# Performance work log

Hardware: AMD Instinct MI355X
Metric: run time of the kernel (lower is better)

The kernel has to match this reference:

```python
import jax, jax.numpy as jnp
import numpy as np

N = 100_000      # nodes
E = 1_600_000    # graph edges
M = 10_000       # hyperedges
I = 800_000      # hypergraph incidences
F_IN = 128
HID = 128


def _lin(key, fan_in, fan_out):
    return (jax.random.normal(key, (fan_in, fan_out), jnp.float32) / np.sqrt(fan_in)).astype(jnp.float32)


def setup_inputs() -> dict:
    key = jax.random.key(0)
    ks = jax.random.split(key, 14)
    x = jax.random.normal(ks[0], (N, F_IN), jnp.float32)
    edge_index = jax.random.randint(ks[1], (2, E), 0, N, dtype=jnp.int32)
    edge_weights = jax.random.uniform(ks[2], (E,), jnp.float32)
    node_idx = jax.random.randint(ks[3], (I,), 0, N, dtype=jnp.int32)
    he_idx = jax.random.randint(ks[4], (I,), 0, M, dtype=jnp.int32)
    hyperedge_index = jnp.stack([node_idx, he_idx])
    hyperedge_distances = jax.random.uniform(ks[5], (M,), jnp.float32)
    return {
        "x": x,
        "edge_index": edge_index,
        "edge_weights": edge_weights,
        "hyperedge_index": hyperedge_index,
        "hyperedge_distances": hyperedge_distances,
        "W_g1": _lin(ks[6], F_IN, HID), "b_g1": jnp.zeros((HID,), jnp.float32),
        "W_g2": _lin(ks[7], HID, HID), "b_g2": jnp.zeros((HID,), jnp.float32),
        "W_h1": _lin(ks[8], F_IN, HID), "b_h1": jnp.zeros((HID,), jnp.float32),
        "W_h2": _lin(ks[9], HID, HID), "b_h2": jnp.zeros((HID,), jnp.float32),
        "W_fc": _lin(ks[10], 2 * HID, HID), "b_fc": jnp.zeros((HID,), jnp.float32),
        "W_out": _lin(ks[11], HID, 2), "b_out": jnp.zeros((2,), jnp.float32),
    }


def _gcn(h_in, W, b, row, col, ew):
    # PyG GCNConv: lin -> sym-normalized scatter-add (self-loops included in row/col/ew) -> +bias
    h = h_in @ W
    deg = jax.ops.segment_sum(ew, col, num_segments=N)
    dis = jnp.where(deg > 0, jax.lax.rsqrt(deg), 0.0)
    norm = dis[row] * ew * dis[col]
    out = jax.ops.segment_sum(norm[:, None] * h[row], col, num_segments=N)
    return out + b


def _hyper(h_in, W, b, node_idx, he_idx):
    # PyG HypergraphConv (use_attention=False, hyperedge_weight=1):
    # out = D^{-1} H B^{-1} H^T (X W) + b
    h = h_in @ W
    D = jax.ops.segment_sum(jnp.ones((node_idx.shape[0],), h.dtype), node_idx, num_segments=N)
    Dinv = jnp.where(D > 0, 1.0 / D, 0.0)
    Bc = jax.ops.segment_sum(jnp.ones((he_idx.shape[0],), h.dtype), he_idx, num_segments=M)
    Binv = jnp.where(Bc > 0, 1.0 / Bc, 0.0)
    edge_feat = Binv[:, None] * jax.ops.segment_sum(h[node_idx], he_idx, num_segments=M)
    out = Dinv[:, None] * jax.ops.segment_sum(edge_feat[he_idx], node_idx, num_segments=N)
    return out + b


def reference(x, edge_index, edge_weights, hyperedge_index, hyperedge_distances,
              W_g1, b_g1, W_g2, b_g2, W_h1, b_h1, W_h2, b_h2,
              W_fc, b_fc, W_out, b_out):
    # add self-loops (GCNConv default add_self_loops=True, fill=1)
    loops = jnp.arange(N, dtype=edge_index.dtype)
    row = jnp.concatenate([edge_index[0], loops])
    col = jnp.concatenate([edge_index[1], loops])
    ew = jnp.concatenate([edge_weights, jnp.ones((N,), edge_weights.dtype)])

    # GCN branch (dropout = identity in eval)
    x1 = jax.nn.relu(_gcn(x, W_g1, b_g1, row, col, ew))
    x1 = jax.nn.relu(_gcn(x1, W_g2, b_g2, row, col, ew))

    # vectorized form of the per-incidence python loop:
    # node_hyperedge_weights[v] = sum over incidences (v, e) of hyperedge_distances[e]
    node_idx, he_idx = hyperedge_index[0], hyperedge_index[1]
    nhw = jax.ops.segment_sum(hyperedge_distances[he_idx], node_idx, num_segments=N)
    x2 = x * nhw[:, None]

    x2 = jax.nn.relu(_hyper(x2, W_h1, b_h1, node_idx, he_idx))
    x2 = jax.nn.relu(_hyper(x2, W_h2, b_h2, node_idx, he_idx))

    h = jnp.concatenate([x1, x2], axis=1)
    h = jax.nn.relu(h @ W_fc + b_fc)
    return h @ W_out + b_out
```

## Files before the change

kernel.cpp:

```cpp
#include <hip/hip_runtime.h>
#include <hip/hip_fp16.h>


#define THREADS 256
#define CAP_E  64
#define CAP_IN 40
#define CAP_IH 144

#define BC_E 4608
#define BC_I 2432
#define BC_H 3072

#define P1_ITEMS 16
#define P1_BLOCK 4096

#define SMEM_MM 50176

typedef _Float16 half8 __attribute__((ext_vector_type(8)));
typedef float floatx4 __attribute__((ext_vector_type(4)));

#define FIX_SCALE 16777216.0f

template <int MODE>
__device__ __forceinline__ void phase1_core(
    int blk, const int* __restrict__ keys, const int* __restrict__ vals,
    const float* __restrict__ wts,
    unsigned long long* __restrict__ buf64, unsigned int* __restrict__ buf32,
    int* __restrict__ bincnt, int nitems, int nbins, int bincap,
    unsigned int* hist, unsigned int* off, unsigned int* gb, unsigned int* wsum,
    unsigned long long* reord, unsigned short* rbin) {
  const int tid = threadIdx.x;
  const int base = blk * P1_BLOCK;
  for (int i = tid; i < 512; i += 256) hist[i] = 0;
  __syncthreads();
  unsigned long long pl[P1_ITEMS];
  int bn[P1_ITEMS], lr[P1_ITEMS];
#pragma unroll
  for (int j = 0; j < P1_ITEMS; ++j) {
    int idx = base + j * 256 + tid;
    bn[j] = -1;
    if (idx < nitems) {
      int k = keys[idx], v = vals[idx];
      if (MODE == 0) {
        bn[j] = k >> 8;
        pl[j] = ((unsigned long long)__float_as_uint(wts[idx]) << 32) |
                ((unsigned long long)((unsigned int)v << 8)) |
                (unsigned long long)(k & 255);
      } else if (MODE == 1) {
        bn[j] = k >> 8;
        pl[j] = (unsigned long long)(((unsigned int)v << 8) | (unsigned int)(k & 255));
      } else {
        bn[j] = k >> 5;
        pl[j] = (unsigned long long)(((unsigned int)v << 5) | (unsigned int)(k & 31));
      }
      lr[j] = (int)atomicAdd(&hist[bn[j]], 1u);
    }
  }
  __syncthreads();
  unsigned int v0 = hist[2 * tid], v1 = hist[2 * tid + 1];
  unsigned int tsum = v0 + v1;
  unsigned int incl = tsum;
  for (int o = 1; o < 64; o <<= 1) {
    unsigned int t = __shfl_up(incl, o, 64);
    if ((tid & 63) >= o) incl += t;
  }
  if ((tid & 63) == 63) wsum[tid >> 6] = incl;
  __syncthreads();
  unsigned int woff = 0;
  for (int w = 0; w < (tid >> 6); ++w) woff += wsum[w];
  unsigned int texcl = incl - tsum + woff;
  off[2 * tid] = texcl;
  off[2 * tid + 1] = texcl + v0;
  if (2 * tid < nbins && v0) gb[2 * tid] = (unsigned int)atomicAdd(&bincnt[2 * tid], (int)v0);
  if (2 * tid + 1 < nbins && v1) gb[2 * tid + 1] = (unsigned int)atomicAdd(&bincnt[2 * tid + 1], (int)v1);
  __syncthreads();
#pragma unroll
  for (int j = 0; j < P1_ITEMS; ++j) {
    if (bn[j] >= 0) {
      unsigned int pos = off[bn[j]] + (unsigned int)lr[j];
      reord[pos] = pl[j];
      rbin[pos] = (unsigned short)bn[j];
    }
  }
  __syncthreads();
  int total = nitems - base;
  if (total > P1_BLOCK) total = P1_BLOCK;
#pragma unroll
  for (int j = 0; j < P1_ITEMS; ++j) {
    int p = j * 256 + tid;
    if (p < total) {
      int b = rbin[p];
      unsigned int idx = gb[b] + (unsigned int)p - off[b];
      if (idx < (unsigned int)bincap) {
        if (MODE == 0) buf64[(size_t)b * bincap + idx] = reord[p];
        else buf32[(size_t)b * bincap + idx] = (unsigned int)reord[p];
      }
    }
  }
}

__global__ __launch_bounds__(256) void bin_phase1_all(
    const int* __restrict__ col, const int* __restrict__ row, const float* __restrict__ ew,
    const int* __restrict__ vidx, const int* __restrict__ heidx,
    unsigned long long* __restrict__ buf_e, unsigned int* __restrict__ buf_in,
    unsigned int* __restrict__ buf_ih,
    int* __restrict__ bincnt_e, int* __restrict__ bincnt_in, int* __restrict__ bincnt_ih,
    int E, int I, int GB_E, int GB_I, int NB_E, int NB_I, int NB_H) {
  __shared__ unsigned int hist[512];
  __shared__ unsigned int off[512];
  __shared__ unsigned int gb[512];
  __shared__ unsigned int wsum[4];
  __shared__ unsigned long long reord[P1_BLOCK];
  __shared__ unsigned short rbin[P1_BLOCK];
  int b = blockIdx.x;
  if (b < GB_E)
    phase1_core<0>(b, col, row, ew, buf_e, nullptr, bincnt_e, E, NB_E, BC_E,
                   hist, off, gb, wsum, reord, rbin);
  else if (b < GB_E + GB_I)
    phase1_core<1>(b - GB_E, vidx, heidx, nullptr, nullptr, buf_in, bincnt_in, I, NB_I, BC_I,
                   hist, off, gb, wsum, reord, rbin);
  else
    phase1_core<2>(b - GB_E - GB_I, heidx, vidx, nullptr, nullptr, buf_ih, bincnt_ih, I, NB_H, BC_H,
                   hist, off, gb, wsum, reord, rbin);
}

__global__ __launch_bounds__(256) void bin_phase2_all(
    const unsigned long long* __restrict__ buf_e, const unsigned int* __restrict__ buf_in,
    const unsigned int* __restrict__ buf_ih,
    const int* __restrict__ bincnt_e, const int* __restrict__ bincnt_in,
    const int* __restrict__ bincnt_ih, const float* __restrict__ hd,
    int2* __restrict__ epairs, int* __restrict__ he_by_node, int* __restrict__ v_by_he,
    int* __restrict__ ecnt, float* __restrict__ dis,
    int* __restrict__ ncnt, float* __restrict__ nhwf, float* __restrict__ Dinv,
    int* __restrict__ hecnt, float* __restrict__ Binv,
    int N, int M, int NB_E, int NB_I) {
  __shared__ unsigned int cnt[256];
  __shared__ unsigned int aux[256];
  const int tid = threadIdx.x;
  int b = blockIdx.x;
  if (b < NB_E) {
    cnt[tid] = 0; aux[tid] = 0;
    __syncthreads();
    int tot = bincnt_e[b]; if (tot > BC_E) tot = BC_E;
    const unsigned long long* seg = buf_e + (size_t)b * BC_E;
    for (int i = tid; i < tot; i += 256) {
      unsigned long long pl = seg[i];
      int c_lo = (int)(pl & 255u);
      int r = (int)((pl >> 8) & 0xFFFFFFu);
      float w = __uint_as_float((unsigned int)(pl >> 32));
      unsigned int s = atomicAdd(&cnt[c_lo], 1u);
      atomicAdd(&aux[c_lo], (unsigned int)(w * FIX_SCALE + 0.5f));
      if (s < CAP_E)
        epairs[((size_t)b * 256 + c_lo) * CAP_E + s] = make_int2(r, __float_as_int(w));
    }
    __syncthreads();
    int v = b * 256 + tid;
    if (v < N) {
      unsigned int c = cnt[tid];
      ecnt[v] = (c < CAP_E) ? (int)c : CAP_E;
      dis[v] = rsqrtf(1.0f + (float)aux[tid] * (1.0f / FIX_SCALE));
    }
  } else if (b < NB_E + NB_I) {
    b -= NB_E;
    cnt[tid] = 0; aux[tid] = 0;
    __syncthreads();
    int tot = bincnt_in[b]; if (tot > BC_I) tot = BC_I;
    const unsigned int* seg = buf_in + (size_t)b * BC_I;
    for (int i = tid; i < tot; i += 256) {
      unsigned int pl = seg[i];
      int v_lo = (int)(pl & 255u);
      int e = (int)(pl >> 8);
      unsigned int s = atomicAdd(&cnt[v_lo], 1u);
      atomicAdd(&aux[v_lo], (unsigned int)(hd[e] * FIX_SCALE + 0.5f));
      if (s < CAP_IN) he_by_node[((size_t)b * 256 + v_lo) * CAP_IN + s] = e;
    }
    __syncthreads();
    int v = b * 256 + tid;
    if (v < N) {
      unsigned int c = cnt[tid];
      ncnt[v] = (c < CAP_IN) ? (int)c : CAP_IN;
      nhwf[v] = (float)aux[tid] * (1.0f / FIX_SCALE);
      Dinv[v] = (c > 0) ? 1.0f / (float)c : 0.0f;
    }
  } else {
    b -= NB_E + NB_I;
    if (tid < 32) cnt[tid] = 0;
    __syncthreads();
    int tot = bincnt_ih[b]; if (tot > BC_H) tot = BC_H;
    const unsigned int* seg = buf_ih + (size_t)b * BC_H;
    for (int i = tid; i < tot; i += 256) {
      unsigned int pl = seg[i];
      int e_lo = (int)(pl & 31u);
      int v = (int)(pl >> 5);
      unsigned int s = atomicAdd(&cnt[e_lo], 1u);
      if (s < CAP_IH) v_by_he[((size_t)b * 32 + e_lo) * CAP_IH + s] = v;
    }
    __syncthreads();
    if (tid < 32) {
      int e = b * 32 + tid;
      if (e < M) {
        unsigned int c = cnt[tid];
        hecnt[e] = (c < CAP_IH) ? (int)c : CAP_IH;
        Binv[e] = (c > 0) ? 1.0f / (float)c : 0.0f;
      }
    }
  }
}

__global__ void prep_k(const float* __restrict__ Wg1, const float* __restrict__ Wg2,
                       const float* __restrict__ Wh1, const float* __restrict__ Wh2,
                       const float* __restrict__ Wfc,
                       _Float16* __restrict__ Wtg1, _Float16* __restrict__ Wtg2,
                       _Float16* __restrict__ Wth1, _Float16* __restrict__ Wth2,
                       _Float16* __restrict__ Wtfc, int* __restrict__ bincnt, int nbins) {
  if (blockIdx.x == gridDim.x - 1) {
    for (int i = threadIdx.x; i < nbins; i += 256) bincnt[i] = 0;
    return;
  }
  int idx = blockIdx.x * THREADS + threadIdx.x;
  if (idx < 65536) {
    int s = idx >> 14, local = idx & 16383;
    const float* W = (s == 0) ? Wg1 : (s == 1) ? Wg2 : (s == 2) ? Wh1 : Wh2;
    _Float16* Wt = (s == 0) ? Wtg1 : (s == 1) ? Wtg2 : (s == 2) ? Wth1 : Wth2;
    int n = local >> 7, kk = local & 127;
    int k = kk ^ ((n & 7) << 3);
    Wt[local] = (_Float16)W[k * 128 + n];
  } else if (idx < 98304) {
    int local = idx - 65536;
    int n = local >> 8, kk = local & 255;
    int k = kk ^ ((n & 7) << 3);
    Wtfc[local] = (_Float16)Wfc[k * 128 + n];
  }
}

__device__ __forceinline__ void mm_core(
    int blk, const _Float16* __restrict__ A, const _Float16* __restrict__ Wt,
    const float* __restrict__ scale, _Float16* __restrict__ Cout, int nrows,
    unsigned char* smem) {
  _Float16* WtL = (_Float16*)smem;
  _Float16* ebuf = (_Float16*)(smem + 32768);
  const int tid = threadIdx.x;
  {
    const float4* src = (const float4*)Wt;
    float4* dst = (float4*)WtL;
#pragma unroll
    for (int i = 0; i < 8; ++i) dst[tid + 256 * i] = src[tid + 256 * i];
  }
  __syncthreads();
  const int w = tid >> 6, l = tid & 63;
  const int m = l & 15, quad = l >> 4;
  const int rbase = blk * 256 + w * 64;
  floatx4 acc[4][8];
#pragma unroll
  for (int r = 0; r < 4; ++r)
#pragma unroll
    for (int c = 0; c < 8; ++c)
#pragma unroll
      for (int j = 0; j < 4; ++j) acc[r][c][j] = 0.0f;
#pragma unroll
  for (int s = 0; s < 4; ++s) {
    const int ks = s * 32 + quad * 8;
    half8 a[4];
#pragma unroll
    for (int r = 0; r < 4; ++r) {
      int gr = rbase + r * 16 + m;
      if (gr < nrows) {
        a[r] = *(const half8*)(A + (size_t)gr * 128 + ks);
      } else {
#pragma unroll
        for (int j = 0; j < 8; ++j) a[r][j] = (_Float16)0.0f;
      }
    }
#pragma unroll
    for (int c = 0; c < 8; ++c) {
      int n = c * 16 + m;
      half8 b = *(const half8*)&WtL[n * 128 + (ks ^ ((n & 7) << 3))];
#pragma unroll
      for (int r = 0; r < 4; ++r)
        acc[r][c] = __builtin_amdgcn_mfma_f32_16x16x32_f16(a[r], b, acc[r][c], 0, 0, 0);
    }
  }
  _Float16* eb = ebuf + w * (16 * 136);
#pragma unroll
  for (int r = 0; r < 4; ++r) {
    float dv[4];
#pragma unroll
    for (int j = 0; j < 4; ++j) {
      int grow = rbase + r * 16 + quad * 4 + j;
      dv[j] = (scale && grow < nrows) ? scale[grow] : 1.0f;
    }
#pragma unroll
    for (int c = 0; c < 8; ++c)
#pragma unroll
      for (int j = 0; j < 4; ++j)
        eb[(quad * 4 + j) * 136 + c * 16 + m] = (_Float16)(acc[r][c][j] * dv[j]);
#pragma unroll
    for (int t = 0; t < 4; ++t) {
      int chunk = t * 64 + l;
      int rr = chunk >> 4;
      int off = (chunk & 15) * 8;
      int gr = rbase + r * 16 + rr;
      half8 v = *(const half8*)&eb[rr * 136 + off];
      if (gr < nrows) *(half8*)(Cout + (size_t)gr * 128 + off) = v;
    }
  }
}

__global__ __launch_bounds__(256) void mm_dual(
    const float* __restrict__ X, const _Float16* __restrict__ Wt1,
    const _Float16* __restrict__ Wt2, _Float16* __restrict__ C1,
    _Float16* __restrict__ C2, int nrows) {
  __shared__ __align__(16) unsigned char smem[SMEM_MM];
  _Float16* WtL = (_Float16*)smem;
  _Float16* ebuf = (_Float16*)(smem + 32768);
  const int tid = threadIdx.x;
  const int w = tid >> 6, l = tid & 63;
  const int m = l & 15, quad = l >> 4;
  const int rbase = blockIdx.x * 256 + w * 64;
  half8 a[4][4];
#pragma unroll
  for (int r = 0; r < 4; ++r) {
    int gr = rbase + r * 16 + m;
#pragma unroll
    for (int s = 0; s < 4; ++s) {
      int ks = s * 32 + quad * 8;
      if (gr < nrows) {
        float4 f0 = *(const float4*)(X + (size_t)gr * 128 + ks);
        float4 f1 = *(const float4*)(X + (size_t)gr * 128 + ks + 4);
        half8 h;
        h[0] = (_Float16)f0.x; h[1] = (_Float16)f0.y; h[2] = (_Float16)f0.z; h[3] = (_Float16)f0.w;
        h[4] = (_Float16)f1.x; h[5] = (_Float16)f1.y; h[6] = (_Float16)f1.z; h[7] = (_Float16)f1.w;
        a[r][s] = h;
      } else {
#pragma unroll
        for (int j = 0; j < 8; ++j) a[r][s][j] = (_Float16)0.0f;
      }
    }
  }
  _Float16* eb = ebuf + w * (16 * 136);
  for (int pass = 0; pass < 2; ++pass) {
    {
      const float4* src = (const float4*)(pass ? Wt2 : Wt1);
      float4* dst = (float4*)WtL;
#pragma unroll
      for (int i = 0; i < 8; ++i) dst[tid + 256 * i] = src[tid + 256 * i];
    }
    __syncthreads();
    floatx4 acc[4][8];
#pragma unroll
    for (int r = 0; r < 4; ++r)
#pragma unroll
      for (int c = 0; c < 8; ++c)
#pragma unroll
        for (int j = 0; j < 4; ++j) acc[r][c][j] = 0.0f;
#pragma unroll
    for (int s = 0; s < 4; ++s) {
      const int ks = s * 32 + quad * 8;
#pragma unroll
      for (int c = 0; c < 8; ++c) {
        int n = c * 16 + m;
        half8 b = *(const half8*)&WtL[n * 128 + (ks ^ ((n & 7) << 3))];
#pragma unroll
        for (int r = 0; r < 4; ++r)
          acc[r][c] = __builtin_amdgcn_mfma_f32_16x16x32_f16(a[r][s], b, acc[r][c], 0, 0, 0);
      }
    }
    _Float16* Cout = pass ? C2 : C1;
#pragma unroll
    for (int r = 0; r < 4; ++r) {
#pragma unroll
      for (int c = 0; c < 8; ++c)
#pragma unroll
        for (int j = 0; j < 4; ++j)
          eb[(quad * 4 + j) * 136 + c * 16 + m] = (_Float16)acc[r][c][j];
#pragma unroll
      for (int t = 0; t < 4; ++t) {
        int chunk = t * 64 + l;
        int rr = chunk >> 4;
        int off = (chunk & 15) * 8;
        int gr = rbase + r * 16 + rr;
        half8 v = *(const half8*)&eb[rr * 136 + off];
        if (gr < nrows) *(half8*)(Cout + (size_t)gr * 128 + off) = v;
      }
    }
    __syncthreads();
  }
}

__global__ __launch_bounds__(256) void mm_pair(
    const _Float16* __restrict__ A1, const _Float16* __restrict__ Wt1,
    const float* __restrict__ scale1, _Float16* __restrict__ C1,
    const _Float16* __restrict__ A2, const _Float16* __restrict__ Wt2,
    _Float16* __restrict__ C2, int nrows, int GMM) {
  __shared__ __align__(16) unsigned char smem[SMEM_MM];
  int b = blockIdx.x;
  if (b < GMM) mm_core(b, A1, Wt1, scale1, C1, nrows, smem);
  else         mm_core(b - GMM, A2, Wt2, nullptr, C2, nrows, smem);
}

template <int PRESCALED>
__device__ __forceinline__ void gcn_core(
    int blk, const _Float16* __restrict__ h, const int* __restrict__ ecnt,
    const int2* __restrict__ epairs, const float* __restrict__ dis,
    const float* __restrict__ bias, _Float16* __restrict__ out, int N) {
  int g = threadIdx.x >> 4, l = threadIdx.x & 15;
  int c = blk * 16 + g;
  if (c >= N) return;
  const float4* h4 = (const float4*)h;
  float dc = dis[c];
  float4 self = h4[(size_t)c * 16 + l];
  const _Float16* sp = (const _Float16*)&self;
  float acc[8];
#pragma unroll
  for (int j = 0; j < 8; ++j) acc[j] = PRESCALED ? (float)sp[j] : dc * (float)sp[j];
  int cnt = ecnt[c];
  const int2* seg = epairs + (size_t)c * CAP_E;
  int p = 0;
  for (; p + 2 <= cnt; p += 2) {
    int2 pr0 = seg[p];
    int2 pr1 = seg[p + 1];
    float4 hv0 = h4[(size_t)pr0.x * 16 + l];
    float4 hv1 = h4[(size_t)pr1.x * 16 + l];
    float w0 = __int_as_float(pr0.y), w1 = __int_as_float(pr1.y);
    if (!PRESCALED) { w0 *= dis[pr0.x]; w1 *= dis[pr1.x]; }
    const _Float16* hp0 = (const _Float16*)&hv0;
    const _Float16* hp1 = (const _Float16*)&hv1;
#pragma unroll
    for (int j = 0; j < 8; ++j) acc[j] = fmaf(w0, (float)hp0[j], acc[j]);
#pragma unroll
    for (int j = 0; j < 8; ++j) acc[j] = fmaf(w1, (float)hp1[j], acc[j]);
  }
  if (p < cnt) {
    int2 pr = seg[p];
    float wgt = __int_as_float(pr.y);
    if (!PRESCALED) wgt *= dis[pr.x];
    float4 hv = h4[(size_t)pr.x * 16 + l];
    const _Float16* hp = (const _Float16*)&hv;
#pragma unroll
    for (int j = 0; j < 8; ++j) acc[j] = fmaf(wgt, (float)hp[j], acc[j]);
  }
  float4 b0 = ((const float4*)bias)[2 * l];
  float4 b1 = ((const float4*)bias)[2 * l + 1];
  float bb[8] = {b0.x, b0.y, b0.z, b0.w, b1.x, b1.y, b1.z, b1.w};
  half8 ov;
#pragma unroll
  for (int j = 0; j < 8; ++j) ov[j] = (_Float16)fmaxf(fmaf(acc[j], dc, bb[j]), 0.f);
  *(half8*)(out + (size_t)c * 128 + l * 8) = ov;
}

template <int SCALED>
__device__ __forceinline__ void hyperef_core(
    int blk, const _Float16* __restrict__ h, const int* __restrict__ hecnt,
    const int* __restrict__ v_by_he, const float* __restrict__ Binv,
    const float* __restrict__ nhwf, _Float16* __restrict__ ef, int M) {
  int g = threadIdx.x >> 4, l = threadIdx.x & 15;
  int e = blk * 16 + g;
  if (e >= M) return;
  const float4* h4 = (const float4*)h;
  float acc[8];
#pragma unroll
  for (int j = 0; j < 8; ++j) acc[j] = 0.f;
  int cnt = hecnt[e];
  const int* seg = v_by_he + (size_t)e * CAP_IH;
  int p = 0;
  for (; p + 4 <= cnt; p += 4) {
    int v0 = seg[p], v1 = seg[p + 1], v2 = seg[p + 2], v3 = seg[p + 3];
    float4 a0 = h4[(size_t)v0 * 16 + l];
    float4 a1 = h4[(size_t)v1 * 16 + l];
    float4 a2 = h4[(size_t)v2 * 16 + l];
    float4 a3 = h4[(size_t)v3 * 16 + l];
    float s0 = 1.f, s1 = 1.f, s2 = 1.f, s3 = 1.f;
    if (SCALED) { s0 = nhwf[v0]; s1 = nhwf[v1]; s2 = nhwf[v2]; s3 = nhwf[v3]; }
    const _Float16* p0 = (const _Float16*)&a0;
    const _Float16* p1 = (const _Float16*)&a1;
    const _Float16* p2 = (const _Float16*)&a2;
    const _Float16* p3 = (const _Float16*)&a3;
    if (SCALED) {
#pragma unroll
      for (int j = 0; j < 8; ++j)
        acc[j] += s0 * (float)p0[j] + s1 * (float)p1[j] + s2 * (float)p2[j] + s3 * (float)p3[j];
    } else {
#pragma unroll
      for (int j = 0; j < 8; ++j)
        acc[j] += ((float)p0[j] + (float)p1[j]) + ((float)p2[j] + (float)p3[j]);
    }
  }
  for (; p < cnt; ++p) {
    int v = seg[p];
    float4 hv = h4[(size_t)v * 16 + l];
    const _Float16* hp = (const _Float16*)&hv;
    if (SCALED) {
      float s = nhwf[v];
#pragma unroll
      for (int j = 0; j < 8; ++j) acc[j] = fmaf(s, (float)hp[j], acc[j]);
    } else {
#pragma unroll
      for (int j = 0; j < 8; ++j) acc[j] += (float)hp[j];
    }
  }
  float bi = Binv[e];
  half8 ov;
#pragma unroll
  for (int j = 0; j < 8; ++j) ov[j] = (_Float16)(acc[j] * bi);
  *(half8*)(ef + (size_t)e * 128 + l * 8) = ov;
}

__global__ __launch_bounds__(256) void g_he_1(
    const _Float16* __restrict__ Bg, const int* __restrict__ ecnt,
    const int2* __restrict__ epairs, const float* __restrict__ dis,
    const float* __restrict__ bg1, _Float16* __restrict__ Bt1,
    const _Float16* __restrict__ Bh, const int* __restrict__ hecnt,
    const int* __restrict__ v_by_he, const float* __restrict__ Binv,
    const float* __restrict__ nhwf, _Float16* __restrict__ ef,
    int N, int M, int GN16) {
  int b = blockIdx.x;
  if (b < GN16) gcn_core<0>(b, Bg, ecnt, epairs, dis, bg1, Bt1, N);
  else hyperef_core<1>(b - GN16, Bh, hecnt, v_by_he, Binv, nhwf, ef, M);
}

__global__ __launch_bounds__(256) void g_he_2(
    const _Float16* __restrict__ Btmp1, const int* __restrict__ ecnt,
    const int2* __restrict__ epairs, const float* __restrict__ dis,
    const float* __restrict__ bg2, _Float16* __restrict__ Bt1,
    const _Float16* __restrict__ Btmp2, const int* __restrict__ hecnt,
    const int* __restrict__ v_by_he, const float* __restrict__ Binv,
    _Float16* __restrict__ ef, int N, int M, int GN16) {
  int b = blockIdx.x;
  if (b < GN16) gcn_core<1>(b, Btmp1, ecnt, epairs, dis, bg2, Bt1, N);
  else hyperef_core<0>(b - GN16, Btmp2, hecnt, v_by_he, Binv, nullptr, ef, M);
}

__global__ __launch_bounds__(256) void hyper_out16(
    const _Float16* __restrict__ ef, const int* __restrict__ ncnt,
    const int* __restrict__ he_by_node, const float* __restrict__ Dinv,
    const float* __restrict__ bias, _Float16* __restrict__ out, int N) {
  int g = threadIdx.x >> 4, l = threadIdx.x & 15;
  int v = blockIdx.x * 16 + g;
  if (v >= N) return;
  const float4* ef4 = (const float4*)ef;
  float acc[8];
#pragma unroll
  for (int j = 0; j < 8; ++j) acc[j] = 0.f;
  int cnt = ncnt[v];
  const int* seg = he_by_node + (size_t)v * CAP_IN;
  int p = 0;
  for (; p + 2 <= cnt; p += 2) {
    int e0 = seg[p], e1 = seg[p + 1];
    float4 a0 = ef4[(size_t)e0 * 16 + l];
    float4 a1 = ef4[(size_t)e1 * 16 + l];
    const _Float16* p0 = (const _Float16*)&a0;
    const _Float16* p1 = (const _Float16*)&a1;
#pragma unroll
    for (int j = 0; j < 8; ++j) acc[j] += (float)p0[j] + (float)p1[j];
  }
  if (p < cnt) {
    int e = seg[p];
    float4 hv = ef4[(size_t)e * 16 + l];
    const _Float16* hp = (const _Float16*)&hv;
#pragma unroll
    for (int j = 0; j < 8; ++j) acc[j] += (float)hp[j];
  }
  float di = Dinv[v];
  float4 b0 = ((const float4*)bias)[2 * l];
  float4 b1 = ((const float4*)bias)[2 * l + 1];
  float bb[8] = {b0.x, b0.y, b0.z, b0.w, b1.x, b1.y, b1.z, b1.w};
  half8 ov;
#pragma unroll
  for (int j = 0; j < 8; ++j) ov[j] = (_Float16)fmaxf(fmaf(acc[j], di, bb[j]), 0.f);
  *(half8*)(out + (size_t)v * 128 + l * 8) = ov;
}

__global__ __launch_bounds__(256) void fc_head(
    const _Float16* __restrict__ A1, const _Float16* __restrict__ A2,
    const _Float16* __restrict__ Wt, const float* __restrict__ bfc,
    const float* __restrict__ Wout, const float* __restrict__ bout,
    float* __restrict__ out, int nrows) {
  __shared__ _Float16 WtL[128 * 128];
  __shared__ float WoutL[256];
  const int tid = threadIdx.x;
  WoutL[tid] = Wout[tid];
  const int w = tid >> 6, l = tid & 63;
  const int m = l & 15, quad = l >> 4;
  const int rbase = blockIdx.x * 256 + w * 64;
  floatx4 acc[4][8];
#pragma unroll
  for (int r = 0; r < 4; ++r)
#pragma unroll
    for (int c = 0; c < 8; ++c)
#pragma unroll
      for (int j = 0; j < 4; ++j) acc[r][c][j] = 0.0f;
  for (int half = 0; half < 2; ++half) {
    {
      const float4* src = (const float4*)Wt;
      float4* dst = (float4*)WtL;
#pragma unroll
      for (int i = 0; i < 8; ++i) {
        int idx = tid + 256 * i;
        dst[idx] = src[(idx >> 4) * 32 + half * 16 + (idx & 15)];
      }
    }
    __syncthreads();
    const _Float16* Asrc = half ? A2 : A1;
#pragma unroll
    for (int ss = 0; ss < 4; ++ss) {
      const int kl = ss * 32 + quad * 8;
      half8 a[4];
#pragma unroll
      for (int r = 0; r < 4; ++r) {
        int gr = rbase + r * 16 + m;
        if (gr < nrows) {
          a[r] = *(const half8*)(Asrc + (size_t)gr * 128 + kl);
        } else {
#pragma unroll
          for (int j = 0; j < 8; ++j) a[r][j] = (_Float16)0.0f;
        }
      }
#pragma unroll
      for (int c = 0; c < 8; ++c) {
        int n = c * 16 + m;
        half8 b = *(const half8*)&WtL[n * 128 + (kl ^ ((n & 7) << 3))];
#pragma unroll
        for (int r = 0; r < 4; ++r)
          acc[r][c] = __builtin_amdgcn_mfma_f32_16x16x32_f16(a[r], b, acc[r][c], 0, 0, 0);
      }
    }
    __syncthreads();
  }
  float b0 = bout[0], b1 = bout[1];
  float bias_c[8];
#pragma unroll
  for (int c = 0; c < 8; ++c) bias_c[c] = bfc[c * 16 + m];
#pragma unroll
  for (int r = 0; r < 4; ++r) {
#pragma unroll
    for (int j = 0; j < 4; ++j) {
      float s0 = 0.f, s1 = 0.f;
#pragma unroll
      for (int c = 0; c < 8; ++c) {
        float h = fmaxf(acc[r][c][j] + bias_c[c], 0.f);
        int k = c * 16 + m;
        s0 = fmaf(h, WoutL[k * 2 + 0], s0);
        s1 = fmaf(h, WoutL[k * 2 + 1], s1);
      }
#pragma unroll
      for (int off = 1; off < 16; off <<= 1) {
        s0 += __shfl_xor(s0, off, 64);
        s1 += __shfl_xor(s1, off, 64);
      }
      if (m == 0) {
        int gr = rbase + r * 16 + quad * 4 + j;
        if (gr < nrows) {
          float2 o = make_float2(s0 + b0, s1 + b1);
          *(float2*)(out + (size_t)gr * 2) = o;
        }
      }
    }
  }
}

extern "C" void kernel_launch(void* const* d_in, const int* in_sizes, int n_in,
                              void* d_out, int out_size, void* d_ws, size_t ws_size,
                              hipStream_t stream) {
  const float* x    = (const float*)d_in[0];
  const int*   eidx = (const int*)d_in[1];
  const float* ew   = (const float*)d_in[2];
  const int*   hidx = (const int*)d_in[3];
  const float* hd   = (const float*)d_in[4];
  const float* Wg1  = (const float*)d_in[5];
  const float* bg1  = (const float*)d_in[6];
  const float* Wg2  = (const float*)d_in[7];
  const float* bg2  = (const float*)d_in[8];
  const float* Wh1  = (const float*)d_in[9];
  const float* bh1  = (const float*)d_in[10];
  const float* Wh2  = (const float*)d_in[11];
  const float* bh2  = (const float*)d_in[12];
  const float* Wfc  = (const float*)d_in[13];
  const float* bfc  = (const float*)d_in[14];
  const float* Wout = (const float*)d_in[15];
  const float* bout = (const float*)d_in[16];

  const int N = in_sizes[0] / 128;
  const int E = in_sizes[2];
  const int I = in_sizes[3] / 2;
  const int M = in_sizes[4];
  const int* row   = eidx;
  const int* col   = eidx + E;
  const int* vidx  = hidx;
  const int* heidx = hidx + I;

  const int NB_E = (N + 255) >> 8;
  const int NB_I = (N + 255) >> 8;
  const int NB_H = (M + 31) >> 5;
  const int GB_E = (E + P1_BLOCK - 1) / P1_BLOCK;
  const int GB_I = (I + P1_BLOCK - 1) / P1_BLOCK;

  char* p = (char*)d_ws;
  auto alloc = [&](size_t bytes) -> void* {
    void* r = (void*)p;
    p += (bytes + 255) & ~(size_t)255;
    return r;
  };
  float* dis   = (float*)alloc((size_t)N * 4);
  float* nhwf  = (float*)alloc((size_t)N * 4);
  float* Dinv  = (float*)alloc((size_t)N * 4);
  float* Binv  = (float*)alloc((size_t)M * 4);
  int* ecnt    = (int*)alloc((size_t)N * 4);
  int* ncnt    = (int*)alloc((size_t)N * 4);
  int* hecnt   = (int*)alloc((size_t)M * 4);
  int* bincnt_e  = (int*)alloc((size_t)(NB_E + NB_I + NB_H) * 4);
  int* bincnt_in = bincnt_e + NB_E;
  int* bincnt_ih = bincnt_in + NB_I;
  int2* epairs = (int2*)alloc((size_t)N * CAP_E * 8);
  int* he_by_node = (int*)alloc((size_t)N * CAP_IN * 4);
  int* v_by_he    = (int*)alloc((size_t)M * CAP_IH * 4);
  _Float16* Bg   = (_Float16*)alloc((size_t)N * 128 * 2);
  _Float16* Bh   = (_Float16*)alloc((size_t)N * 128 * 2);
  _Float16* Bt1  = (_Float16*)alloc((size_t)N * 128 * 2);
  _Float16* Bt2  = (_Float16*)alloc((size_t)N * 128 * 2);
  _Float16* ef16 = (_Float16*)alloc((size_t)M * 128 * 2);
  _Float16* Wtg1 = (_Float16*)alloc(128 * 128 * 2);
  _Float16* Wtg2 = (_Float16*)alloc(128 * 128 * 2);
  _Float16* Wth1 = (_Float16*)alloc(128 * 128 * 2);
  _Float16* Wth2 = (_Float16*)alloc(128 * 128 * 2);
  _Float16* Wtfc = (_Float16*)alloc(128 * 256 * 2);

  unsigned long long* buf_e  = (unsigned long long*)Bt1;
  unsigned int*       buf_in = (unsigned int*)Bt2;
  unsigned int*       buf_ih = (unsigned int*)((char*)Bt2 + (4 << 20));

  const int GMM  = (N + 255) / 256;
  const int GN16 = (N + 15) / 16;
  const int GM16 = (M + 15) / 16;
  const int NBINS = NB_E + NB_I + NB_H;

  prep_k<<<385, THREADS, 0, stream>>>(Wg1, Wg2, Wh1, Wh2, Wfc,
                                      Wtg1, Wtg2, Wth1, Wth2, Wtfc, bincnt_e, NBINS);
  bin_phase1_all<<<GB_E + 2 * GB_I, THREADS, 0, stream>>>(
      col, row, ew, vidx, heidx, buf_e, buf_in, buf_ih,
      bincnt_e, bincnt_in, bincnt_ih, E, I, GB_E, GB_I, NB_E, NB_I, NB_H);
  bin_phase2_all<<<NBINS, THREADS, 0, stream>>>(
      buf_e, buf_in, buf_ih, bincnt_e, bincnt_in, bincnt_ih, hd,
      epairs, he_by_node, v_by_he, ecnt, dis, ncnt, nhwf, Dinv, hecnt, Binv,
      N, M, NB_E, NB_I);
  mm_dual<<<GMM, THREADS, 0, stream>>>(x, Wtg1, Wth1, Bg, Bh, N);
  g_he_1<<<GN16 + GM16, THREADS, 0, stream>>>(
      Bg, ecnt, epairs, dis, bg1, Bt1,
      Bh, hecnt, v_by_he, Binv, nhwf, ef16, N, M, GN16);
  hyper_out16<<<GN16, THREADS, 0, stream>>>(ef16, ncnt, he_by_node, Dinv, bh1, Bt2, N);
  mm_pair<<<2 * GMM, THREADS, 0, stream>>>(Bt1, Wtg2, dis, Bg, Bt2, Wth2, Bh, N, GMM);
  g_he_2<<<GN16 + GM16, THREADS, 0, stream>>>(
      Bg, ecnt, epairs, dis, bg2, Bt1,
      Bh, hecnt, v_by_he, Binv, ef16, N, M, GN16);
  hyper_out16<<<GN16, THREADS, 0, stream>>>(ef16, ncnt, he_by_node, Dinv, bh2, Bt2, N);
  fc_head<<<GMM, THREADS, 0, stream>>>(Bt1, Bt2, Wtfc, bfc, Wout, bout, (float*)d_out, N);
}
```

Baseline: 523.5 us.

## Restructure kernel schedule: fold prescaling into GEMM, merge prep and fuse hyper-out with GEMM

Folds the dis and nhwf row scaling into the first dual GEMM epilogue, so both gather kernels handle prescaled inputs and no longer need per-neighbor scale loads. The weight-prep kernel is merged into the binning phase-1 launch, and the bin-count zeroing moves to hipMemsetAsync. The first hyperedge output and the second GCN GEMM now run in one launch; this splits the old mm_pair, so the hyper second-layer GEMM becomes a separate mm_single launch. GEMM shared memory is reused for the epilogue staging buffer (with an added barrier), which lowers LDS use, and the gather loops are unrolled wider with vectorised index loads. This risks more sequential dependencies between launches and adds an extra fp16 rounding of the scaled values.

```diff
diff --git a/kernel.cpp b/kernel.cpp
--- a/kernel.cpp
+++ b/kernel.cpp
@@ -13,8 +13,6 @@
 
 #define P1_ITEMS 16
 #define P1_BLOCK 4096
-
-#define SMEM_MM 50176
 
 typedef _Float16 half8 __attribute__((ext_vector_type(8)));
 typedef float floatx4 __attribute__((ext_vector_type(4)));
@@ -99,13 +97,19 @@
   }
 }
 
-__global__ __launch_bounds__(256) void bin_phase1_all(
+__global__ __launch_bounds__(256) void prep_phase1(
     const int* __restrict__ col, const int* __restrict__ row, const float* __restrict__ ew,
     const int* __restrict__ vidx, const int* __restrict__ heidx,
     unsigned long long* __restrict__ buf_e, unsigned int* __restrict__ buf_in,
     unsigned int* __restrict__ buf_ih,
     int* __restrict__ bincnt_e, int* __restrict__ bincnt_in, int* __restrict__ bincnt_ih,
-    int E, int I, int GB_E, int GB_I, int NB_E, int NB_I, int NB_H) {
+    int E, int I, int GB_E, int GB_I, int NB_E, int NB_I, int NB_H,
+    const float* __restrict__ Wg1, const float* __restrict__ Wg2,
+    const float* __restrict__ Wh1, const float* __restrict__ Wh2,
+    const float* __restrict__ Wfc,
+    _Float16* __restrict__ Wtg1, _Float16* __restrict__ Wtg2,
+    _Float16* __restrict__ Wth1, _Float16* __restrict__ Wth2,
+    _Float16* __restrict__ Wtfc) {
   __shared__ unsigned int hist[512];
   __shared__ unsigned int off[512];
   __shared__ unsigned int gb[512];
@@ -113,15 +117,32 @@
   __shared__ unsigned long long reord[P1_BLOCK];
   __shared__ unsigned short rbin[P1_BLOCK];
   int b = blockIdx.x;
-  if (b < GB_E)
+  const int GBtot = GB_E + 2 * GB_I;
+  if (b < GB_E) {
     phase1_core<0>(b, col, row, ew, buf_e, nullptr, bincnt_e, E, NB_E, BC_E,
                    hist, off, gb, wsum, reord, rbin);
-  else if (b < GB_E + GB_I)
+  } else if (b < GB_E + GB_I) {
     phase1_core<1>(b - GB_E, vidx, heidx, nullptr, nullptr, buf_in, bincnt_in, I, NB_I, BC_I,
                    hist, off, gb, wsum, reord, rbin);
-  else
+  } else if (b < GBtot) {
     phase1_core<2>(b - GB_E - GB_I, heidx, vidx, nullptr, nullptr, buf_ih, bincnt_ih, I, NB_H, BC_H,
                    hist, off, gb, wsum, reord, rbin);
+  } else {
+    int idx = (b - GBtot) * THREADS + threadIdx.x;
+    if (idx < 65536) {
+      int s = idx >> 14, local = idx & 16383;
+      const float* W = (s == 0) ? Wg1 : (s == 1) ? Wg2 : (s == 2) ? Wh1 : Wh2;
+      _Float16* Wt = (s == 0) ? Wtg1 : (s == 1) ? Wtg2 : (s == 2) ? Wth1 : Wth2;
+      int n = local >> 7, kk = local & 127;
+      int k = kk ^ ((n & 7) << 3);
+      Wt[local] = (_Float16)W[k * 128 + n];
+    } else if (idx < 98304) {
+      int local = idx - 65536;
+      int n = local >> 8, kk = local & 255;
+      int k = kk ^ ((n & 7) << 3);
+      Wtfc[local] = (_Float16)Wfc[k * 128 + n];
+    }
+  }
 }
 
 __global__ __launch_bounds__(256) void bin_phase2_all(
@@ -207,38 +228,10 @@
   }
 }
 
-__global__ void prep_k(const float* __restrict__ Wg1, const float* __restrict__ Wg2,
-                       const float* __restrict__ Wh1, const float* __restrict__ Wh2,
-                       const float* __restrict__ Wfc,
-                       _Float16* __restrict__ Wtg1, _Float16* __restrict__ Wtg2,
-                       _Float16* __restrict__ Wth1, _Float16* __restrict__ Wth2,
-                       _Float16* __restrict__ Wtfc, int* __restrict__ bincnt, int nbins) {
-  if (blockIdx.x == gridDim.x - 1) {
-    for (int i = threadIdx.x; i < nbins; i += 256) bincnt[i] = 0;
-    return;
-  }
-  int idx = blockIdx.x * THREADS + threadIdx.x;
-  if (idx < 65536) {
-    int s = idx >> 14, local = idx & 16383;
-    const float* W = (s == 0) ? Wg1 : (s == 1) ? Wg2 : (s == 2) ? Wh1 : Wh2;
-    _Float16* Wt = (s == 0) ? Wtg1 : (s == 1) ? Wtg2 : (s == 2) ? Wth1 : Wth2;
-    int n = local >> 7, kk = local & 127;
-    int k = kk ^ ((n & 7) << 3);
-    Wt[local] = (_Float16)W[k * 128 + n];
-  } else if (idx < 98304) {
-    int local = idx - 65536;
-    int n = local >> 8, kk = local & 255;
-    int k = kk ^ ((n & 7) << 3);
-    Wtfc[local] = (_Float16)Wfc[k * 128 + n];
-  }
-}
-
 __device__ __forceinline__ void mm_core(
     int blk, const _Float16* __restrict__ A, const _Float16* __restrict__ Wt,
     const float* __restrict__ scale, _Float16* __restrict__ Cout, int nrows,
-    unsigned char* smem) {
-  _Float16* WtL = (_Float16*)smem;
-  _Float16* ebuf = (_Float16*)(smem + 32768);
+    _Float16* WtL) {
   const int tid = threadIdx.x;
   {
     const float4* src = (const float4*)Wt;
@@ -280,7 +273,8 @@
         acc[r][c] = __builtin_amdgcn_mfma_f32_16x16x32_f16(a[r], b, acc[r][c], 0, 0, 0);
     }
   }
-  _Float16* eb = ebuf + w * (16 * 136);
+  __syncthreads();
+  _Float16* eb = WtL + w * (16 * 136);
 #pragma unroll
   for (int r = 0; r < 4; ++r) {
     float dv[4];
@@ -308,11 +302,10 @@
 
 __global__ __launch_bounds__(256) void mm_dual(
     const float* __restrict__ X, const _Float16* __restrict__ Wt1,
-    const _Float16* __restrict__ Wt2, _Float16* __restrict__ C1,
+    const _Float16* __restrict__ Wt2, const float* __restrict__ dis,
+    const float* __restrict__ nhwf, _Float16* __restrict__ C1,
     _Float16* __restrict__ C2, int nrows) {
-  __shared__ __align__(16) unsigned char smem[SMEM_MM];
-  _Float16* WtL = (_Float16*)smem;
-  _Float16* ebuf = (_Float16*)(smem + 32768);
+  __shared__ _Float16 WtL[128 * 128];
   const int tid = threadIdx.x;
   const int w = tid >> 6, l = tid & 63;
   const int m = l & 15, quad = l >> 4;
@@ -337,7 +330,6 @@
       }
     }
   }
-  _Float16* eb = ebuf + w * (16 * 136);
   for (int pass = 0; pass < 2; ++pass) {
     {
       const float4* src = (const float4*)(pass ? Wt2 : Wt1);
@@ -365,14 +357,23 @@
           acc[r][c] = __builtin_amdgcn_mfma_f32_16x16x32_f16(a[r][s], b, acc[r][c], 0, 0, 0);
       }
     }
+    __syncthreads();
+    const float* scale = pass ? nhwf : dis;
     _Float16* Cout = pass ? C2 : C1;
+    _Float16* eb = WtL + w * (16 * 136);
 #pragma unroll
     for (int r = 0; r < 4; ++r) {
+      float dv[4];
+#pragma unroll
+      for (int j = 0; j < 4; ++j) {
+        int grow = rbase + r * 16 + quad * 4 + j;
+        dv[j] = (grow < nrows) ? scale[grow] : 1.0f;
+      }
 #pragma unroll
       for (int c = 0; c < 8; ++c)
 #pragma unroll
         for (int j = 0; j < 4; ++j)
-          eb[(quad * 4 + j) * 136 + c * 16 + m] = (_Float16)acc[r][c][j];
+          eb[(quad * 4 + j) * 136 + c * 16 + m] = (_Float16)(acc[r][c][j] * dv[j]);
 #pragma unroll
       for (int t = 0; t < 4; ++t) {
         int chunk = t * 64 + l;
@@ -387,18 +388,6 @@
   }
 }
 
-__global__ __launch_bounds__(256) void mm_pair(
-    const _Float16* __restrict__ A1, const _Float16* __restrict__ Wt1,
-    const float* __restrict__ scale1, _Float16* __restrict__ C1,
-    const _Float16* __restrict__ A2, const _Float16* __restrict__ Wt2,
-    _Float16* __restrict__ C2, int nrows, int GMM) {
-  __shared__ __align__(16) unsigned char smem[SMEM_MM];
-  int b = blockIdx.x;
-  if (b < GMM) mm_core(b, A1, Wt1, scale1, C1, nrows, smem);
-  else         mm_core(b - GMM, A2, Wt2, nullptr, C2, nrows, smem);
-}
-
-template <int PRESCALED>
 __device__ __forceinline__ void gcn_core(
     int blk, const _Float16* __restrict__ h, const int* __restrict__ ecnt,
     const int2* __restrict__ epairs, const float* __restrict__ dis,
@@ -407,38 +396,43 @@
   int c = blk * 16 + g;
   if (c >= N) return;
   const float4* h4 = (const float4*)h;
-  float dc = dis[c];
   float4 self = h4[(size_t)c * 16 + l];
   const _Float16* sp = (const _Float16*)&self;
   float acc[8];
 #pragma unroll
-  for (int j = 0; j < 8; ++j) acc[j] = PRESCALED ? (float)sp[j] : dc * (float)sp[j];
+  for (int j = 0; j < 8; ++j) acc[j] = (float)sp[j];
   int cnt = ecnt[c];
   const int2* seg = epairs + (size_t)c * CAP_E;
   int p = 0;
-  for (; p + 2 <= cnt; p += 2) {
-    int2 pr0 = seg[p];
-    int2 pr1 = seg[p + 1];
-    float4 hv0 = h4[(size_t)pr0.x * 16 + l];
-    float4 hv1 = h4[(size_t)pr1.x * 16 + l];
-    float w0 = __int_as_float(pr0.y), w1 = __int_as_float(pr1.y);
-    if (!PRESCALED) { w0 *= dis[pr0.x]; w1 *= dis[pr1.x]; }
+  for (; p + 4 <= cnt; p += 4) {
+    int4 pa = *(const int4*)&seg[p];
+    int4 pb = *(const int4*)&seg[p + 2];
+    float4 hv0 = h4[(size_t)pa.x * 16 + l];
+    float4 hv1 = h4[(size_t)pa.z * 16 + l];
+    float4 hv2 = h4[(size_t)pb.x * 16 + l];
+    float4 hv3 = h4[(size_t)pb.z * 16 + l];
+    float w0 = __int_as_float(pa.y), w1 = __int_as_float(pa.w);
+    float w2 = __int_as_float(pb.y), w3 = __int_as_float(pb.w);
     const _Float16* hp0 = (const _Float16*)&hv0;
     const _Float16* hp1 = (const _Float16*)&hv1;
-#pragma unroll
-    for (int j = 0; j < 8; ++j) acc[j] = fmaf(w0, (float)hp0[j], acc[j]);
-#pragma unroll
-    for (int j = 0; j < 8; ++j) acc[j] = fmaf(w1, (float)hp1[j], acc[j]);
-  }
-  if (p < cnt) {
+    const _Float16* hp2 = (const _Float16*)&hv2;
+    const _Float16* hp3 = (const _Float16*)&hv3;
+#pragma unroll
+    for (int j = 0; j < 8; ++j) {
+      float t0 = fmaf(w0, (float)hp0[j], w1 * (float)hp1[j]);
+      float t1 = fmaf(w2, (float)hp2[j], w3 * (float)hp3[j]);
+      acc[j] += t0 + t1;
+    }
+  }
+  for (; p < cnt; ++p) {
     int2 pr = seg[p];
     float wgt = __int_as_float(pr.y);
-    if (!PRESCALED) wgt *= dis[pr.x];
     float4 hv = h4[(size_t)pr.x * 16 + l];
     const _Float16* hp = (const _Float16*)&hv;
 #pragma unroll
     for (int j = 0; j < 8; ++j) acc[j] = fmaf(wgt, (float)hp[j], acc[j]);
   }
+  float dc = dis[c];
   float4 b0 = ((const float4*)bias)[2 * l];
   float4 b1 = ((const float4*)bias)[2 * l + 1];
   float bb[8] = {b0.x, b0.y, b0.z, b0.w, b1.x, b1.y, b1.z, b1.w};
@@ -448,11 +442,10 @@
   *(half8*)(out + (size_t)c * 128 + l * 8) = ov;
 }
 
-template <int SCALED>
 __device__ __forceinline__ void hyperef_core(
     int blk, const _Float16* __restrict__ h, const int* __restrict__ hecnt,
     const int* __restrict__ v_by_he, const float* __restrict__ Binv,
-    const float* __restrict__ nhwf, _Float16* __restrict__ ef, int M) {
+    _Float16* __restrict__ ef, int M) {
   int g = threadIdx.x >> 4, l = threadIdx.x & 15;
   int e = blk * 16 + g;
   if (e >= M) return;
@@ -463,40 +456,52 @@
   int cnt = hecnt[e];
   const int* seg = v_by_he + (size_t)e * CAP_IH;
   int p = 0;
-  for (; p + 4 <= cnt; p += 4) {
-    int v0 = seg[p], v1 = seg[p + 1], v2 = seg[p + 2], v3 = seg[p + 3];
-    float4 a0 = h4[(size_t)v0 * 16 + l];
-    float4 a1 = h4[(size_t)v1 * 16 + l];
-    float4 a2 = h4[(size_t)v2 * 16 + l];
-    float4 a3 = h4[(size_t)v3 * 16 + l];
-    float s0 = 1.f, s1 = 1.f, s2 = 1.f, s3 = 1.f;
-    if (SCALED) { s0 = nhwf[v0]; s1 = nhwf[v1]; s2 = nhwf[v2]; s3 = nhwf[v3]; }
+  for (; p + 8 <= cnt; p += 8) {
+    int4 va = *(const int4*)&seg[p];
+    int4 vb = *(const int4*)&seg[p + 4];
+    float4 a0 = h4[(size_t)va.x * 16 + l];
+    float4 a1 = h4[(size_t)va.y * 16 + l];
+    float4 a2 = h4[(size_t)va.z * 16 + l];
+    float4 a3 = h4[(size_t)va.w * 16 + l];
+    float4 a4 = h4[(size_t)vb.x * 16 + l];
+    float4 a5 = h4[(size_t)vb.y * 16 + l];
+    float4 a6 = h4[(size_t)vb.z * 16 + l];
+    float4 a7 = h4[(size_t)vb.w * 16 + l];
     const _Float16* p0 = (const _Float16*)&a0;
     const _Float16* p1 = (const _Float16*)&a1;
     const _Float16* p2 = (const _Float16*)&a2;
     const _Float16* p3 = (const _Float16*)&a3;
-    if (SCALED) {
-#pragma unroll
-      for (int j = 0; j < 8; ++j)
-        acc[j] += s0 * (float)p0[j] + s1 * (float)p1[j] + s2 * (float)p2[j] + s3 * (float)p3[j];
-    } else {
-#pragma unroll
-      for (int j = 0; j < 8; ++j)
-        acc[j] += ((float)p0[j] + (float)p1[j]) + ((float)p2[j] + (float)p3[j]);
-    }
+    const _Float16* p4 = (const _Float16*)&a4;
+    const _Float16* p5 = (const _Float16*)&a5;
+    const _Float16* p6 = (const _Float16*)&a6;
+    const _Float16* p7 = (const _Float16*)&a7;
+#pragma unroll
+    for (int j = 0; j < 8; ++j) {
+      float t0 = ((float)p0[j] + (float)p1[j]) + ((float)p2[j] + (float)p3[j]);
+      float t1 = ((float)p4[j] + (float)p5[j]) + ((float)p6[j] + (float)p7[j]);
+      acc[j] += t0 + t1;
+    }
+  }
+  for (; p + 4 <= cnt; p += 4) {
+    int4 va = *(const int4*)&seg[p];
+    float4 a0 = h4[(size_t)va.x * 16 + l];
+    float4 a1 = h4[(size_t)va.y * 16 + l];
+    float4 a2 = h4[(size_t)va.z * 16 + l];
+    float4 a3 = h4[(size_t)va.w * 16 + l];
+    const _Float16* p0 = (const _Float16*)&a0;
+    const _Float16* p1 = (const _Float16*)&a1;
+    const _Float16* p2 = (const _Float16*)&a2;
+    const _Float16* p3 = (const _Float16*)&a3;
+#pragma unroll
+    for (int j = 0; j < 8; ++j)
+      acc[j] += ((float)p0[j] + (float)p1[j]) + ((float)p2[j] + (float)p3[j]);
   }
   for (; p < cnt; ++p) {
     int v = seg[p];
     float4 hv = h4[(size_t)v * 16 + l];
     const _Float16* hp = (const _Float16*)&hv;
-    if (SCALED) {
-      float s = nhwf[v];
-#pragma unroll
-      for (int j = 0; j < 8; ++j) acc[j] = fmaf(s, (float)hp[j], acc[j]);
-    } else {
-#pragma unroll
-      for (int j = 0; j < 8; ++j) acc[j] += (float)hp[j];
-    }
+#pragma unroll
+    for (int j = 0; j < 8; ++j) acc[j] += (float)hp[j];
   }
   float bi = Binv[e];
   half8 ov;
@@ -505,37 +510,24 @@
   *(half8*)(ef + (size_t)e * 128 + l * 8) = ov;
 }
 
-__global__ __launch_bounds__(256) void g_he_1(
+__global__ __launch_bounds__(256) void g_he(
     const _Float16* __restrict__ Bg, const int* __restrict__ ecnt,
     const int2* __restrict__ epairs, const float* __restrict__ dis,
-    const float* __restrict__ bg1, _Float16* __restrict__ Bt1,
+    const float* __restrict__ bias_g, _Float16* __restrict__ Bt1,
     const _Float16* __restrict__ Bh, const int* __restrict__ hecnt,
-    const int* __restrict__ v_by_he, const float* __restrict__ Binv,
-    const float* __restrict__ nhwf, _Float16* __restrict__ ef,
-    int N, int M, int GN16) {
-  int b = blockIdx.x;
-  if (b < GN16) gcn_core<0>(b, Bg, ecnt, epairs, dis, bg1, Bt1, N);
-  else hyperef_core<1>(b - GN16, Bh, hecnt, v_by_he, Binv, nhwf, ef, M);
-}
-
-__global__ __launch_bounds__(256) void g_he_2(
-    const _Float16* __restrict__ Btmp1, const int* __restrict__ ecnt,
-    const int2* __restrict__ epairs, const float* __restrict__ dis,
-    const float* __restrict__ bg2, _Float16* __restrict__ Bt1,
-    const _Float16* __restrict__ Btmp2, const int* __restrict__ hecnt,
     const int* __restrict__ v_by_he, const float* __restrict__ Binv,
     _Float16* __restrict__ ef, int N, int M, int GN16) {
   int b = blockIdx.x;
-  if (b < GN16) gcn_core<1>(b, Btmp1, ecnt, epairs, dis, bg2, Bt1, N);
-  else hyperef_core<0>(b - GN16, Btmp2, hecnt, v_by_he, Binv, nullptr, ef, M);
-}
-
-__global__ __launch_bounds__(256) void hyper_out16(
-    const _Float16* __restrict__ ef, const int* __restrict__ ncnt,
+  if (b < GN16) gcn_core(b, Bg, ecnt, epairs, dis, bias_g, Bt1, N);
+  else hyperef_core(b - GN16, Bh, hecnt, v_by_he, Binv, ef, M);
+}
+
+__device__ __forceinline__ void ho_core(
+    int blk, const _Float16* __restrict__ ef, const int* __restrict__ ncnt,
     const int* __restrict__ he_by_node, const float* __restrict__ Dinv,
     const float* __restrict__ bias, _Float16* __restrict__ out, int N) {
   int g = threadIdx.x >> 4, l = threadIdx.x & 15;
-  int v = blockIdx.x * 16 + g;
+  int v = blk * 16 + g;
   if (v >= N) return;
   const float4* ef4 = (const float4*)ef;
   float acc[8];
@@ -544,16 +536,21 @@
   int cnt = ncnt[v];
   const int* seg = he_by_node + (size_t)v * CAP_IN;
   int p = 0;
-  for (; p + 2 <= cnt; p += 2) {
-    int e0 = seg[p], e1 = seg[p + 1];
-    float4 a0 = ef4[(size_t)e0 * 16 + l];
-    float4 a1 = ef4[(size_t)e1 * 16 + l];
+  for (; p + 4 <= cnt; p += 4) {
+    int4 ea = *(const int4*)&seg[p];
+    float4 a0 = ef4[(size_t)ea.x * 16 + l];
+    float4 a1 = ef4[(size_t)ea.y * 16 + l];
+    float4 a2 = ef4[(size_t)ea.z * 16 + l];
+    float4 a3 = ef4[(size_t)ea.w * 16 + l];
     const _Float16* p0 = (const _Float16*)&a0;
     const _Float16* p1 = (const _Float16*)&a1;
-#pragma unroll
-    for (int j = 0; j < 8; ++j) acc[j] += (float)p0[j] + (float)p1[j];
-  }
-  if (p < cnt) {
+    const _Float16* p2 = (const _Float16*)&a2;
+    const _Float16* p3 = (const _Float16*)&a3;
+#pragma unroll
+    for (int j = 0; j < 8; ++j)
+      acc[j] += ((float)p0[j] + (float)p1[j]) + ((float)p2[j] + (float)p3[j]);
+  }
+  for (; p < cnt; ++p) {
     int e = seg[p];
     float4 hv = ef4[(size_t)e * 16 + l];
     const _Float16* hp = (const _Float16*)&hv;
@@ -568,6 +565,33 @@
 #pragma unroll
   for (int j = 0; j < 8; ++j) ov[j] = (_Float16)fmaxf(fmaf(acc[j], di, bb[j]), 0.f);
   *(half8*)(out + (size_t)v * 128 + l * 8) = ov;
+}
+
+__global__ __launch_bounds__(256) void ho_mmg2(
+    const _Float16* __restrict__ ef, const int* __restrict__ ncnt,
+    const int* __restrict__ he_by_node, const float* __restrict__ Dinv,
+    const float* __restrict__ bh1, _Float16* __restrict__ Bt2,
+    const _Float16* __restrict__ Bt1, const _Float16* __restrict__ Wtg2,
+    const float* __restrict__ dis, _Float16* __restrict__ Bg,
+    int N, int GN16) {
+  __shared__ _Float16 WtL[128 * 128];
+  int b = blockIdx.x;
+  if (b < GN16) ho_core(b, ef, ncnt, he_by_node, Dinv, bh1, Bt2, N);
+  else mm_core(b - GN16, Bt1, Wtg2, dis, Bg, N, WtL);
+}
+
+__global__ __launch_bounds__(256) void mm_single(
+    const _Float16* __restrict__ A, const _Float16* __restrict__ Wt,
+    _Float16* __restrict__ C, int nrows) {
+  __shared__ _Float16 WtL[128 * 128];
+  mm_core(blockIdx.x, A, Wt, nullptr, C, nrows, WtL);
+}
+
+__global__ __launch_bounds__(256) void hyper_out16(
+    const _Float16* __restrict__ ef, const int* __restrict__ ncnt,
+    const int* __restrict__ he_by_node, const float* __restrict__ Dinv,
+    const float* __restrict__ bias, _Float16* __restrict__ out, int N) {
+  ho_core(blockIdx.x, ef, ncnt, he_by_node, Dinv, bias, out, N);
 }
 
 __global__ __launch_bounds__(256) void fc_head(
@@ -732,25 +756,25 @@
   const int GN16 = (N + 15) / 16;
   const int GM16 = (M + 15) / 16;
   const int NBINS = NB_E + NB_I + NB_H;
-
-  prep_k<<<385, THREADS, 0, stream>>>(Wg1, Wg2, Wh1, Wh2, Wfc,
-                                      Wtg1, Wtg2, Wth1, Wth2, Wtfc, bincnt_e, NBINS);
-  bin_phase1_all<<<GB_E + 2 * GB_I, THREADS, 0, stream>>>(
+  const int GBtot = GB_E + 2 * GB_I;
+
+  hipMemsetAsync(bincnt_e, 0, (size_t)NBINS * 4, stream);
+  prep_phase1<<<GBtot + 384, THREADS, 0, stream>>>(
       col, row, ew, vidx, heidx, buf_e, buf_in, buf_ih,
-      bincnt_e, bincnt_in, bincnt_ih, E, I, GB_E, GB_I, NB_E, NB_I, NB_H);
+      bincnt_e, bincnt_in, bincnt_ih, E, I, GB_E, GB_I, NB_E, NB_I, NB_H,
+      Wg1, Wg2, Wh1, Wh2, Wfc, Wtg1, Wtg2, Wth1, Wth2, Wtfc);
   bin_phase2_all<<<NBINS, THREADS, 0, stream>>>(
       buf_e, buf_in, buf_ih, bincnt_e, bincnt_in, bincnt_ih, hd,
       epairs, he_by_node, v_by_he, ecnt, dis, ncnt, nhwf, Dinv, hecnt, Binv,
       N, M, NB_E, NB_I);
-  mm_dual<<<GMM, THREADS, 0, stream>>>(x, Wtg1, Wth1, Bg, Bh, N);
-  g_he_1<<<GN16 + GM16, THREADS, 0, stream>>>(
-      Bg, ecnt, epairs, dis, bg1, Bt1,
-      Bh, hecnt, v_by_he, Binv, nhwf, ef16, N, M, GN16);
-  hyper_out16<<<GN16, THREADS, 0, stream>>>(ef16, ncnt, he_by_node, Dinv, bh1, Bt2, N);
-  mm_pair<<<2 * GMM, THREADS, 0, stream>>>(Bt1, Wtg2, dis, Bg, Bt2, Wth2, Bh, N, GMM);
-  g_he_2<<<GN16 + GM16, THREADS, 0, stream>>>(
-      Bg, ecnt, epairs, dis, bg2, Bt1,
-      Bh, hecnt, v_by_he, Binv, ef16, N, M, GN16);
+  mm_dual<<<GMM, THREADS, 0, stream>>>(x, Wtg1, Wth1, dis, nhwf, Bg, Bh, N);
+  g_he<<<GN16 + GM16, THREADS, 0, stream>>>(
+      Bg, ecnt, epairs, dis, bg1, Bt1, Bh, hecnt, v_by_he, Binv, ef16, N, M, GN16);
+  ho_mmg2<<<GN16 + GMM, THREADS, 0, stream>>>(
+      ef16, ncnt, he_by_node, Dinv, bh1, Bt2, Bt1, Wtg2, dis, Bg, N, GN16);
+  mm_single<<<GMM, THREADS, 0, stream>>>(Bt2, Wth2, Bh, N);
+  g_he<<<GN16 + GM16, THREADS, 0, stream>>>(
+      Bg, ecnt, epairs, dis, bg2, Bt1, Bh, hecnt, v_by_he, Binv, ef16, N, M, GN16);
   hyper_out16<<<GN16, THREADS, 0, stream>>>(ef16, ncnt, he_by_node, Dinv, bh2, Bt2, N);
   fc_head<<<GMM, THREADS, 0, stream>>>(Bt1, Bt2, Wtfc, bfc, Wout, bout, (float*)d_out, N);
 }
```

Result: slower. 538.7 us (+2.9%).
